# Optimization experiments

Measured on AMD Instinct MI355X. Metric: run time of the kernel, lower is better.

Reference implementation:

```python
import jax, jax.numpy as jnp
import numpy as np

B, DIM, H, W = 8, 512, 32, 32
NUM_HEADS, KEY_DIM, VALUE_DIM, DIM_OUT = 8, 64, 64, 512


def setup_inputs() -> dict:
    key = jax.random.key(0)
    ks = jax.random.split(key, 5)
    return {
        "x": jax.random.normal(ks[0], (B, DIM, H, W), dtype=jnp.float32),
        "query_proj": jax.random.normal(ks[1], (NUM_HEADS, KEY_DIM, DIM), dtype=jnp.float32),
        "key_proj": jax.random.normal(ks[2], (DIM, KEY_DIM), dtype=jnp.float32),
        "value_proj": jax.random.normal(ks[3], (DIM, VALUE_DIM), dtype=jnp.float32),
        "out_proj": jax.random.normal(ks[4], (DIM_OUT, NUM_HEADS, VALUE_DIM), dtype=jnp.float32),
    }


def reference(x, query_proj, key_proj, value_proj, out_proj):
    b, d, h, w = x.shape
    key_dim = query_proj.shape[1]
    scale = key_dim ** (-0.5)
    # flatten spatial dims to tokens: [b, n, d] where n = h*w (m == x here)
    rx = jnp.transpose(x.reshape(b, d, h * w), (0, 2, 1))
    q = jnp.einsum('bnd,hkd->bnhk', rx, query_proj)
    k = jnp.einsum('bmd,dk->bmk', rx, key_proj)          # single shared K head
    attn = jax.nn.softmax(jnp.einsum('bnhk,bmk->bnhm', q, k) * scale, axis=-1)
    v = jnp.einsum('bmd,dv->bmv', rx, value_proj)        # single shared V head
    o = jnp.einsum('bnhm,bmv->bnhv', attn, v)
    result = jnp.einsum('bnhv,dhv->bdn', o, out_proj)
    return result.reshape(b, -1, h, w)
```

## Files before the change

kernel.cpp:

```cpp
#include <hip/hip_runtime.h>
#include <math.h>

#define BATCH 8
#define DIMD  512
#define NTOK  1024
#define NH    8
#define CQKV  640
#define DOUT  512

typedef __attribute__((ext_vector_type(8))) short short8;
typedef __attribute__((ext_vector_type(4))) short short4v;
typedef __attribute__((ext_vector_type(4))) float f32x4;

__device__ __forceinline__ short bf16rn(float x) {
    unsigned u = __float_as_uint(x);
    u += 0x7FFF + ((u >> 16) & 1);
    return (short)(u >> 16);
}
__device__ __forceinline__ float bf16tof(short s) {
    return __uint_as_float(((unsigned)(unsigned short)s) << 16);
}
struct HL { short h, l; };
__device__ __forceinline__ HL bf16split(float x) {
    HL r;
    r.h = bf16rn(x);
    r.l = bf16rn(x - bf16tof(r.h));
    return r;
}
__device__ __forceinline__ void dma16(const short* g, short* l) {
    __builtin_amdgcn_global_load_lds(
        (const __attribute__((address_space(1))) unsigned int*)g,
        (__attribute__((address_space(3))) unsigned int*)l, 16, 0, 0);
}
__device__ __forceinline__ unsigned packbf2(float f0, float f1) {
    return __builtin_amdgcn_perm(__float_as_uint(f1), __float_as_uint(f0), 0x07060302);
}

#if defined(__has_builtin)
#if __has_builtin(__builtin_amdgcn_mfma_f32_16x16x16bf16_1k)
#define HAVE_MFMA16_BUILTIN 1
__device__ __forceinline__ f32x4 mfma16(short4v a, short4v b, f32x4 c) {
    return __builtin_amdgcn_mfma_f32_16x16x16bf16_1k(a, b, c, 0, 0, 0);
}
#elif __has_builtin(__builtin_amdgcn_mfma_f32_16x16x16_bf16)
#define HAVE_MFMA16_BUILTIN 1
__device__ __forceinline__ f32x4 mfma16(short4v a, short4v b, f32x4 c) {
    return __builtin_amdgcn_mfma_f32_16x16x16_bf16(a, b, c, 0, 0, 0);
}
#endif
#endif
#ifndef HAVE_MFMA16_BUILTIN
__device__ __forceinline__ f32x4 mfma16(short4v a, short4v b, f32x4 c) {
    asm("s_nop 1\n\tv_mfma_f32_16x16x16_bf16 %0, %1, %2, %0"
        : "+v"(c) : "v"(a), "v"(b));
    return c;
}
#endif


__global__ __launch_bounds__(256) void prepack_all(const float* __restrict__ x,
                                                   const float* __restrict__ qp,
                                                   const float* __restrict__ kp,
                                                   const float* __restrict__ vp,
                                                   const float* __restrict__ wout,
                                                   short* __restrict__ whi,
                                                   short* __restrict__ wlo,
                                                   short* __restrict__ xhi,
                                                   short* __restrict__ xlo,
                                                   short* __restrict__ wof) {
    __shared__ float Cs[64][65];
    const int blk = blockIdx.x;
    const int t = threadIdx.x;
    if (blk < 1024) {
        const int nt = blk & 15, dt = (blk >> 4) & 7, b = blk >> 7;
        #pragma unroll
        for (int i = 0; i < 4; ++i) {
            int row = (t >> 4) + i * 16;
            float4 v = *(const float4*)(x + ((size_t)(b * DIMD + dt * 64 + row)) * NTOK
                                          + nt * 64 + (t & 15) * 4);
            Cs[row][(t & 15) * 4 + 0] = v.x;
            Cs[row][(t & 15) * 4 + 1] = v.y;
            Cs[row][(t & 15) * 4 + 2] = v.z;
            Cs[row][(t & 15) * 4 + 3] = v.w;
        }
        __syncthreads();
        for (int u = t; u < 512; u += 256) {
            int lane2 = u & 63, cidx = u >> 6;
            int q2 = lane2 >> 4, r2 = lane2 & 15;
            int kt_loc = cidx & 1, mt_loc = cidx >> 1;
            short8 h8, l8;
            #pragma unroll
            for (int j = 0; j < 8; ++j) {
                HL s = bf16split(Cs[kt_loc * 32 + q2 * 8 + j][mt_loc * 16 + r2]);
                h8[j] = s.h; l8[j] = s.l;
            }
            size_t off = (((size_t)(b * 64 + nt * 4 + mt_loc)) * 16 + dt * 2 + kt_loc) * 512
                         + lane2 * 8;
            *(short8*)&xhi[off] = h8;
            *(short8*)&xlo[off] = l8;
        }
    } else if (blk < 1184) {
        int tid = (blk - 1024) * 256 + t;
        int lane = tid & 63, kt = (tid >> 6) & 15, ct = tid >> 10;
        int q = lane >> 4, r = lane & 15;
        int c = ct * 16 + r;
        short8 h, l;
        #pragma unroll
        for (int j = 0; j < 8; ++j) {
            int d = kt * 32 + q * 8 + j;
            float v;
            if (c < 64)       v = kp[d * 64 + c];
            else if (c < 128) v = vp[d * 64 + (c - 64)];
            else              v = qp[(size_t)(c - 128) * DIMD + d];
            HL s = bf16split(v);
            h[j] = s.h; l[j] = s.l;
        }
        *(short8*)&whi[(size_t)tid * 8] = h;
        *(short8*)&wlo[(size_t)tid * 8] = l;
    } else {
        int tid = (blk - 1184) * 256 + t;
        int lane = tid & 63, kt = (tid >> 6) & 15, mt = tid >> 10;
        int q = lane >> 4, r = lane & 15;
        const float* src = wout + (size_t)(mt * 16 + r) * DOUT + kt * 32 + q * 8;
        short8 h;
        #pragma unroll
        for (int j = 0; j < 8; ++j) h[j] = bf16rn(src[j]);
        *(short8*)&wof[(size_t)tid * 8] = h;
    }
}

__global__ __launch_bounds__(256) void qkv_gemm(const short* __restrict__ xhi,
                                                const short* __restrict__ xlo,
                                                const short* __restrict__ whi,
                                                const short* __restrict__ wlo,
                                                short* __restrict__ khi,
                                                short* __restrict__ klo,
                                                short* __restrict__ vf,
                                                short* __restrict__ qhi,
                                                short* __restrict__ qlo) {
    __shared__ __align__(16) char pool[49152];
    short* Ah = (short*)pool;
    short* Al = Ah + 8192;
    short* Bh = Al + 8192;
    short* Bl = Bh + 4096;
    float (*Cs)[65] = (float(*)[65])pool;

    const int idx = blockIdx.x;
    const int low = idx & 7, rest = idx >> 3;
    const int cb = rest % 10, gh = rest / 10;
    const int g = gh * 8 + low;
    const int b = g >> 3, bml = g & 7;

    const int tid = threadIdx.x, w = tid >> 6, lane = tid & 63;
    const int q = lane >> 4, r = lane & 15;
    f32x4 acc[2][4];
    #pragma unroll
    for (int i = 0; i < 2; ++i)
        #pragma unroll
        for (int j = 0; j < 4; ++j) acc[i][j] = (f32x4){0.f, 0.f, 0.f, 0.f};

    for (int it = 0; it < 8; ++it) {
        __syncthreads();
        for (int u = w; u < 16; u += 4) {
            size_t ga = ((size_t)((b * 64 + bml * 8 + (u >> 1)) * 16 + it * 2 + (u & 1))) * 512 + lane * 8;
            dma16(xhi + ga, &Ah[u * 512]);
            dma16(xlo + ga, &Al[u * 512]);
            if (u < 8) {
                size_t gb = ((size_t)((cb * 4 + (u >> 1)) * 16 + it * 2 + (u & 1))) * 512 + lane * 8;
                dma16(whi + gb, &Bh[u * 512]);
                dma16(wlo + gb, &Bl[u * 512]);
            }
        }
        __syncthreads();
        #pragma unroll
        for (int kc = 0; kc < 2; ++kc) {
            short8 ah[2], al[2];
            #pragma unroll
            for (int rt = 0; rt < 2; ++rt) {
                ah[rt] = *(short8*)&Ah[((w * 2 + rt) * 2 + kc) * 512 + lane * 8];
                al[rt] = *(short8*)&Al[((w * 2 + rt) * 2 + kc) * 512 + lane * 8];
            }
            #pragma unroll
            for (int tt = 0; tt < 4; ++tt) {
                short8 bh = *(short8*)&Bh[(tt * 2 + kc) * 512 + lane * 8];
                short8 bl = *(short8*)&Bl[(tt * 2 + kc) * 512 + lane * 8];
                #pragma unroll
                for (int rt = 0; rt < 2; ++rt) {
                    acc[rt][tt] = __builtin_amdgcn_mfma_f32_16x16x32_bf16(ah[rt], bh, acc[rt][tt], 0, 0, 0);
                    acc[rt][tt] = __builtin_amdgcn_mfma_f32_16x16x32_bf16(ah[rt], bl, acc[rt][tt], 0, 0, 0);
                    acc[rt][tt] = __builtin_amdgcn_mfma_f32_16x16x32_bf16(al[rt], bh, acc[rt][tt], 0, 0, 0);
                }
            }
        }
    }

    __syncthreads();
    #pragma unroll
    for (int rt = 0; rt < 2; ++rt)
        #pragma unroll
        for (int reg = 0; reg < 4; ++reg)
            #pragma unroll
            for (int tt = 0; tt < 4; ++tt)
                Cs[w * 32 + rt * 16 + q * 4 + reg][tt * 16 + r] = acc[rt][tt][reg];
    __syncthreads();

    if (cb == 0) {
        for (int u = tid; u < 1024; u += 256) {
            int lane2 = u & 63, ic = (u >> 6) & 7, tl = u >> 9;
            int q2 = lane2 >> 4, r2 = lane2 & 15;
            int i = ic >> 1, cc = ic & 1;
            short8 h8, l8;
            #pragma unroll
            for (int j = 0; j < 8; ++j) {
                HL s = bf16split(Cs[tl * 64 + i * 16 + r2][cc * 32 + q2 * 8 + j]);
                h8[j] = s.h; l8[j] = s.l;
            }
            size_t off = ((size_t)(b * 16 + bml * 2 + tl) * 8 + ic) * 512 + lane2 * 8;
            *(short8*)&khi[off] = h8;
            *(short8*)&klo[off] = l8;
        }
    } else if (cb == 1) {
        for (int u = tid; u < 1024; u += 256) {
            int lane2 = u & 63, ic = (u >> 6) & 7, tl = u >> 9;
            int q2 = lane2 >> 4, r2 = lane2 & 15;
            int tv = ic >> 1, cc = ic & 1;
            short8 v8;
            #pragma unroll
            for (int j = 0; j < 8; ++j)
                v8[j] = bf16rn(Cs[tl * 64 + cc * 32 + q2 * 8 + j][tv * 16 + r2]);
            size_t off = ((size_t)(b * 16 + bml * 2 + tl) * 8 + ic) * 512 + lane2 * 8;
            *(short8*)&vf[off] = v8;
        }
    } else {
        const int hd = cb - 2;
        const float qscale = 0.125f * 1.44269504f;
        for (int u = tid; u < 1024; u += 256) {
            int lane2 = u & 63, ch = u >> 6;
            int q2 = lane2 >> 4, r2 = lane2 & 15;
            int kc = ch & 1, ntl = ch >> 1;
            short8 h8, l8;
            #pragma unroll
            for (int j = 0; j < 8; ++j) {
                HL s = bf16split(Cs[ntl * 16 + r2][kc * 32 + q2 * 8 + j] * qscale);
                h8[j] = s.h; l8[j] = s.l;
            }
            size_t off = ((((size_t)(b * 8 + hd) * 64 + bml * 8 + ntl) * 2 + kc) * 64 + lane2) * 8;
            *(short8*)&qhi[off] = h8;
            *(short8*)&qlo[off] = l8;
        }
    }
}

__global__ __launch_bounds__(512) void attn_mfma(const short* __restrict__ qhi_g,
                                                 const short* __restrict__ qlo_g,
                                                 const short* __restrict__ khi_g,
                                                 const short* __restrict__ klo_g,
                                                 const short* __restrict__ vf_g,
                                                 short* __restrict__ ob) {
    __shared__ short Khi[2][4096], Klo[2][4096], Vf[2][4096];
    const int blk = blockIdx.x;
    const int b   = blk & 7;
    const int h   = (blk >> 3) & 7;
    const int qt  = blk >> 6;
    const int tid = threadIdx.x;
    const int w    = tid >> 6;
    const int lane = tid & 63;
    const int q    = lane >> 4;
    const int r    = lane & 15;
    const int nt = qt * 8 + w;

    short8 qhi[2], qlo[2];
    #pragma unroll
    for (int c = 0; c < 2; ++c) {
        size_t off = ((((size_t)(b * 8 + h) * 64 + nt) * 2 + c) * 64 + lane) * 8;
        qhi[c] = *(const short8*)&qhi_g[off];
        qlo[c] = *(const short8*)&qlo_g[off];
    }

    short4v bones4;
    #pragma unroll
    for (int j = 0; j < 4; ++j) bones4[j] = (short)0x3F80;

    f32x4 oacc[4], lacc;
    #pragma unroll
    for (int tt = 0; tt < 4; ++tt) oacc[tt] = (f32x4){0.f, 0.f, 0.f, 0.f};
    lacc = (f32x4){0.f, 0.f, 0.f, 0.f};
    float m_ = -1e30f;

    const int kbase = lane * 8;
    const int vbase = ((q >> 1) * 16 + r) * 8 + (q & 1) * 4;

    {
        const size_t kb = ((size_t)(b * 16 + 0) * 8) * 512;
        dma16(khi_g + kb + w * 512 + lane * 8, &Khi[0][w * 512]);
        dma16(klo_g + kb + w * 512 + lane * 8, &Klo[0][w * 512]);
        dma16(vf_g  + kb + w * 512 + lane * 8, &Vf [0][w * 512]);
    }

    for (int t = 0; t < 16; ++t) {
        const int cur = t & 1;
        __builtin_amdgcn_sched_barrier(0);
        asm volatile("s_waitcnt vmcnt(0) lgkmcnt(0)" ::: "memory");
        __builtin_amdgcn_sched_barrier(0);
        __syncthreads();
        if (t < 15) {
            const size_t kb = ((size_t)(b * 16 + t + 1) * 8) * 512;
            dma16(khi_g + kb + w * 512 + lane * 8, &Khi[cur ^ 1][w * 512]);
            dma16(klo_g + kb + w * 512 + lane * 8, &Klo[cur ^ 1][w * 512]);
            dma16(vf_g  + kb + w * 512 + lane * 8, &Vf [cur ^ 1][w * 512]);
        }

        f32x4 sT[4];
        #pragma unroll
        for (int i = 0; i < 4; ++i) sT[i] = (f32x4){0.f, 0.f, 0.f, 0.f};
        #pragma unroll
        for (int cc = 0; cc < 2; ++cc) {
            #pragma unroll
            for (int i = 0; i < 4; ++i) {
                short8 kh = *(short8*)&Khi[cur][(i * 2 + cc) * 512 + kbase];
                short8 kl = *(short8*)&Klo[cur][(i * 2 + cc) * 512 + kbase];
                sT[i] = __builtin_amdgcn_mfma_f32_16x16x32_bf16(kh, qhi[cc], sT[i], 0, 0, 0);
                sT[i] = __builtin_amdgcn_mfma_f32_16x16x32_bf16(kl, qhi[cc], sT[i], 0, 0, 0);
                sT[i] = __builtin_amdgcn_mfma_f32_16x16x32_bf16(kh, qlo[cc], sT[i], 0, 0, 0);
            }
        }

        float pm;
        {
            float a0 = fmaxf(fmaxf(sT[0][0], sT[0][1]), fmaxf(sT[0][2], sT[0][3]));
            float a1 = fmaxf(fmaxf(sT[1][0], sT[1][1]), fmaxf(sT[1][2], sT[1][3]));
            float a2 = fmaxf(fmaxf(sT[2][0], sT[2][1]), fmaxf(sT[2][2], sT[2][3]));
            float a3 = fmaxf(fmaxf(sT[3][0], sT[3][1]), fmaxf(sT[3][2], sT[3][3]));
            pm = fmaxf(fmaxf(a0, a1), fmaxf(a2, a3));
        }
        bool need = (pm > m_ + 30.f);
        if (__any((int)need)) {
            float full = fmaxf(pm, __shfl_xor(pm, 16));
            full = fmaxf(full, __shfl_xor(full, 32));
            float nm = fmaxf(m_, full);
            float alpha = exp2f(m_ - nm);
            m_ = nm;
            #pragma unroll
            for (int reg = 0; reg < 4; ++reg) {
                float areg = __shfl(alpha, q * 20 + reg);
                lacc[reg] *= areg;
                #pragma unroll
                for (int tt = 0; tt < 4; ++tt) oacc[tt][reg] *= areg;
            }
        }
        #pragma unroll
        for (int i = 0; i < 4; ++i)
            #pragma unroll
            for (int reg = 0; reg < 4; ++reg)
                sT[i][reg] = exp2f(sT[i][reg] - m_);

        #pragma unroll
        for (int c = 0; c < 4; ++c) {
            union { uint2 u; short4v s; } pk;
            pk.u.x = packbf2(sT[c][0], sT[c][1]);
            pk.u.y = packbf2(sT[c][2], sT[c][3]);
            short4v pf = pk.s;
            lacc = mfma16(pf, bones4, lacc);
            #pragma unroll
            for (int tt = 0; tt < 4; ++tt) {
                short4v vfr = *(const short4v*)
                    &Vf[cur][vbase + (tt * 2 + (c >> 1)) * 512 + (c & 1) * 256];
                oacc[tt] = mfma16(pf, vfr, oacc[tt]);
            }
        }
    }

    asm volatile("s_nop 7\n\ts_nop 7" :::);

    #pragma unroll
    for (int reg = 0; reg < 4; ++reg) {
        float inv = 1.f / lacc[reg];
        #pragma unroll
        for (int tt = 0; tt < 4; ++tt) {
            int ct = h * 2 + (tt >> 1);
            int lanep = ((tt & 1) * 2 + (r >> 3)) * 16 + q * 4 + reg;
            ob[((((size_t)b * 64 + nt) * 16 + ct) * 64 + lanep) * 8 + (r & 7)] =
                bf16rn(oacc[tt][reg] * inv);
        }
    }
}

__global__ __launch_bounds__(256) void out_gemm(const short* __restrict__ wof,
                                                const short* __restrict__ obf,
                                                float* __restrict__ out) {
    __shared__ short Ah[2][4096];
    __shared__ short Bh[2][4096];
    const int b = blockIdx.z, bd = blockIdx.y, bn = blockIdx.x;
    const int tid = threadIdx.x, w = tid >> 6, lane = tid & 63;
    const int q = lane >> 4, r = lane & 15;
    f32x4 acc[4];
    #pragma unroll
    for (int j = 0; j < 4; ++j) acc[j] = (f32x4){0.f, 0.f, 0.f, 0.f};

    for (int u = w; u < 8; u += 4) {
        size_t ga = ((size_t)((bd * 4 + (u >> 1)) * 16 + (u & 1))) * 512 + lane * 8;
        dma16(wof + ga, &Ah[0][u * 512]);
        size_t gb = ((size_t)((b * 64 + bn * 4 + (u >> 1)) * 16 + (u & 1))) * 512 + lane * 8;
        dma16(obf + gb, &Bh[0][u * 512]);
    }

    for (int it = 0; it < 8; ++it) {
        const int cur = it & 1;
        __syncthreads();
        if (it < 7) {
            for (int u = w; u < 8; u += 4) {
                size_t ga = ((size_t)((bd * 4 + (u >> 1)) * 16 + (it + 1) * 2 + (u & 1))) * 512 + lane * 8;
                dma16(wof + ga, &Ah[cur ^ 1][u * 512]);
                size_t gb = ((size_t)((b * 64 + bn * 4 + (u >> 1)) * 16 + (it + 1) * 2 + (u & 1))) * 512 + lane * 8;
                dma16(obf + gb, &Bh[cur ^ 1][u * 512]);
            }
        }
        #pragma unroll
        for (int kc = 0; kc < 2; ++kc) {
            short8 a = *(short8*)&Ah[cur][(w * 2 + kc) * 512 + lane * 8];
            #pragma unroll
            for (int tt = 0; tt < 4; ++tt) {
                short8 bb = *(short8*)&Bh[cur][(tt * 2 + kc) * 512 + lane * 8];
                acc[tt] = __builtin_amdgcn_mfma_f32_16x16x32_bf16(a, bb, acc[tt], 0, 0, 0);
            }
        }
    }
    const int d_base = bd * 64 + w * 16;
    #pragma unroll
    for (int reg = 0; reg < 4; ++reg)
        #pragma unroll
        for (int tt = 0; tt < 4; ++tt)
            out[((size_t)b * DOUT + d_base + q * 4 + reg) * NTOK
                + bn * 64 + tt * 16 + r] = acc[tt][reg];
}

extern "C" void kernel_launch(void* const* d_in, const int* in_sizes, int n_in,
                              void* d_out, int out_size, void* d_ws, size_t ws_size,
                              hipStream_t stream) {
    const float* x  = (const float*)d_in[0];
    const float* qp = (const float*)d_in[1];
    const float* kp = (const float*)d_in[2];
    const float* vp = (const float*)d_in[3];
    const float* op = (const float*)d_in[4];
    float* out = (float*)d_out;

    short* Whi = (short*)d_ws;
    short* Wlo = Whi + 327680;
    short* Xhi = Wlo + 327680;
    short* Xlo = Xhi + 4194304;
    short* Qhi = Xlo + 4194304;
    short* Qlo = Qhi + 4194304;
    short* Khi = Qlo + 4194304;
    short* Klo = Khi + 524288;
    short* Vf  = Klo + 524288;
    short* Wof = Vf  + 524288;
    short* Ob  = Xhi;

    prepack_all <<<1312, 256, 0, stream>>>(x, qp, kp, vp, op,
                                           Whi, Wlo, Xhi, Xlo, Wof);
    qkv_gemm    <<<640, 256, 0, stream>>>(Xhi, Xlo, Whi, Wlo,
                                          Khi, Klo, Vf, Qhi, Qlo);
    attn_mfma   <<<512, 512, 0, stream>>>(Qhi, Qlo, Khi, Klo, Vf, Ob);
    out_gemm    <<<dim3(16, 8, BATCH), 256, 0, stream>>>(Wof, Ob, out);
}
```

Baseline: 155.4 us.

## Process two query tiles per wave in attention and relayout V fragments

The attention kernel now uses 4 waves per block, each handling two 16-row query tiles, so every K and V fragment read from LDS is reused across two sets of MFMAs. The V prepack layout is changed to a contiguous 256-element-per-fragment format, which lets a single lane-linear short4 load feed the PV MFMA. This halves LDS traffic per unit of work and cuts block-level sync overhead. In exchange it roughly doubles accumulator register pressure, may lower occupancy, and gives each block fewer waves to hide DMA latency.

After: 159.6 us. 2.7% more time.

```diff
diff --git a/kernel.cpp b/kernel.cpp
--- a/kernel.cpp
+++ b/kernel.cpp
@@ -221,14 +221,16 @@
         }
     } else if (cb == 1) {
         for (int u = tid; u < 1024; u += 256) {
-            int lane2 = u & 63, ic = (u >> 6) & 7, tl = u >> 9;
-            int q2 = lane2 >> 4, r2 = lane2 & 15;
-            int tv = ic >> 1, cc = ic & 1;
+            int a = u & 31, ic = (u >> 5) & 15, tl = u >> 9;
+            int c4 = ic >> 2, tv = ic & 3;
             short8 v8;
             #pragma unroll
-            for (int j = 0; j < 8; ++j)
-                v8[j] = bf16rn(Cs[tl * 64 + cc * 32 + q2 * 8 + j][tv * 16 + r2]);
-            size_t off = ((size_t)(b * 16 + bml * 2 + tl) * 8 + ic) * 512 + lane2 * 8;
+            for (int jj = 0; jj < 8; ++jj) {
+                int lane2 = a * 2 + (jj >> 2), j = jj & 3;
+                int qn = lane2 >> 4, r2 = lane2 & 15;
+                v8[jj] = bf16rn(Cs[tl * 64 + c4 * 16 + qn * 4 + j][tv * 16 + r2]);
+            }
+            size_t off = ((size_t)(b * 16 + bml * 2 + tl) * 16 + ic) * 256 + a * 8;
             *(short8*)&vf[off] = v8;
         }
     } else {
@@ -251,7 +253,7 @@
     }
 }
 
-__global__ __launch_bounds__(512) void attn_mfma(const short* __restrict__ qhi_g,
+__global__ __launch_bounds__(256) void attn_mfma(const short* __restrict__ qhi_g,
                                                  const short* __restrict__ qlo_g,
                                                  const short* __restrict__ khi_g,
                                                  const short* __restrict__ klo_g,
@@ -267,34 +269,45 @@
     const int lane = tid & 63;
     const int q    = lane >> 4;
     const int r    = lane & 15;
-    const int nt = qt * 8 + w;
-
-    short8 qhi[2], qlo[2];
-    #pragma unroll
-    for (int c = 0; c < 2; ++c) {
-        size_t off = ((((size_t)(b * 8 + h) * 64 + nt) * 2 + c) * 64 + lane) * 8;
-        qhi[c] = *(const short8*)&qhi_g[off];
-        qlo[c] = *(const short8*)&qlo_g[off];
+
+    short8 qhi[2][2], qlo[2][2];
+    #pragma unroll
+    for (int rt = 0; rt < 2; ++rt) {
+        const int nt = qt * 8 + w * 2 + rt;
+        #pragma unroll
+        for (int c = 0; c < 2; ++c) {
+            size_t off = ((((size_t)(b * 8 + h) * 64 + nt) * 2 + c) * 64 + lane) * 8;
+            qhi[rt][c] = *(const short8*)&qhi_g[off];
+            qlo[rt][c] = *(const short8*)&qlo_g[off];
+        }
     }
 
     short4v bones4;
     #pragma unroll
     for (int j = 0; j < 4; ++j) bones4[j] = (short)0x3F80;
 
-    f32x4 oacc[4], lacc;
-    #pragma unroll
-    for (int tt = 0; tt < 4; ++tt) oacc[tt] = (f32x4){0.f, 0.f, 0.f, 0.f};
-    lacc = (f32x4){0.f, 0.f, 0.f, 0.f};
-    float m_ = -1e30f;
+    f32x4 oacc[2][4], lacc[2];
+    float m_[2];
+    #pragma unroll
+    for (int rt = 0; rt < 2; ++rt) {
+        #pragma unroll
+        for (int tt = 0; tt < 4; ++tt) oacc[rt][tt] = (f32x4){0.f, 0.f, 0.f, 0.f};
+        lacc[rt] = (f32x4){0.f, 0.f, 0.f, 0.f};
+        m_[rt] = -1e30f;
+    }
 
     const int kbase = lane * 8;
-    const int vbase = ((q >> 1) * 16 + r) * 8 + (q & 1) * 4;
+    const int vbase = lane * 4;
 
     {
         const size_t kb = ((size_t)(b * 16 + 0) * 8) * 512;
-        dma16(khi_g + kb + w * 512 + lane * 8, &Khi[0][w * 512]);
-        dma16(klo_g + kb + w * 512 + lane * 8, &Klo[0][w * 512]);
-        dma16(vf_g  + kb + w * 512 + lane * 8, &Vf [0][w * 512]);
+        #pragma unroll
+        for (int ch0 = 0; ch0 < 2; ++ch0) {
+            int ch = w + ch0 * 4;
+            dma16(khi_g + kb + ch * 512 + lane * 8, &Khi[0][ch * 512]);
+            dma16(klo_g + kb + ch * 512 + lane * 8, &Klo[0][ch * 512]);
+            dma16(vf_g  + kb + ch * 512 + lane * 8, &Vf [0][ch * 512]);
+        }
     }
 
     for (int t = 0; t < 16; ++t) {
@@ -305,67 +318,87 @@
         __syncthreads();
         if (t < 15) {
             const size_t kb = ((size_t)(b * 16 + t + 1) * 8) * 512;
-            dma16(khi_g + kb + w * 512 + lane * 8, &Khi[cur ^ 1][w * 512]);
-            dma16(klo_g + kb + w * 512 + lane * 8, &Klo[cur ^ 1][w * 512]);
-            dma16(vf_g  + kb + w * 512 + lane * 8, &Vf [cur ^ 1][w * 512]);
-        }
-
-        f32x4 sT[4];
-        #pragma unroll
-        for (int i = 0; i < 4; ++i) sT[i] = (f32x4){0.f, 0.f, 0.f, 0.f};
+            #pragma unroll
+            for (int ch0 = 0; ch0 < 2; ++ch0) {
+                int ch = w + ch0 * 4;
+                dma16(khi_g + kb + ch * 512 + lane * 8, &Khi[cur ^ 1][ch * 512]);
+                dma16(klo_g + kb + ch * 512 + lane * 8, &Klo[cur ^ 1][ch * 512]);
+                dma16(vf_g  + kb + ch * 512 + lane * 8, &Vf [cur ^ 1][ch * 512]);
+            }
+        }
+
+        f32x4 sT[2][4];
+        #pragma unroll
+        for (int rt = 0; rt < 2; ++rt)
+            #pragma unroll
+            for (int i = 0; i < 4; ++i) sT[rt][i] = (f32x4){0.f, 0.f, 0.f, 0.f};
         #pragma unroll
         for (int cc = 0; cc < 2; ++cc) {
             #pragma unroll
             for (int i = 0; i < 4; ++i) {
                 short8 kh = *(short8*)&Khi[cur][(i * 2 + cc) * 512 + kbase];
                 short8 kl = *(short8*)&Klo[cur][(i * 2 + cc) * 512 + kbase];
-                sT[i] = __builtin_amdgcn_mfma_f32_16x16x32_bf16(kh, qhi[cc], sT[i], 0, 0, 0);
-                sT[i] = __builtin_amdgcn_mfma_f32_16x16x32_bf16(kl, qhi[cc], sT[i], 0, 0, 0);
-                sT[i] = __builtin_amdgcn_mfma_f32_16x16x32_bf16(kh, qlo[cc], sT[i], 0, 0, 0);
-            }
-        }
-
-        float pm;
-        {
-            float a0 = fmaxf(fmaxf(sT[0][0], sT[0][1]), fmaxf(sT[0][2], sT[0][3]));
-            float a1 = fmaxf(fmaxf(sT[1][0], sT[1][1]), fmaxf(sT[1][2], sT[1][3]));
-            float a2 = fmaxf(fmaxf(sT[2][0], sT[2][1]), fmaxf(sT[2][2], sT[2][3]));
-            float a3 = fmaxf(fmaxf(sT[3][0], sT[3][1]), fmaxf(sT[3][2], sT[3][3]));
-            pm = fmaxf(fmaxf(a0, a1), fmaxf(a2, a3));
-        }
-        bool need = (pm > m_ + 30.f);
+                #pragma unroll
+                for (int rt = 0; rt < 2; ++rt) {
+                    sT[rt][i] = __builtin_amdgcn_mfma_f32_16x16x32_bf16(kh, qhi[rt][cc], sT[rt][i], 0, 0, 0);
+                    sT[rt][i] = __builtin_amdgcn_mfma_f32_16x16x32_bf16(kl, qhi[rt][cc], sT[rt][i], 0, 0, 0);
+                    sT[rt][i] = __builtin_amdgcn_mfma_f32_16x16x32_bf16(kh, qlo[rt][cc], sT[rt][i], 0, 0, 0);
+                }
+            }
+        }
+
+        float pm[2];
+        #pragma unroll
+        for (int rt = 0; rt < 2; ++rt) {
+            float a0 = fmaxf(fmaxf(sT[rt][0][0], sT[rt][0][1]), fmaxf(sT[rt][0][2], sT[rt][0][3]));
+            float a1 = fmaxf(fmaxf(sT[rt][1][0], sT[rt][1][1]), fmaxf(sT[rt][1][2], sT[rt][1][3]));
+            float a2 = fmaxf(fmaxf(sT[rt][2][0], sT[rt][2][1]), fmaxf(sT[rt][2][2], sT[rt][2][3]));
+            float a3 = fmaxf(fmaxf(sT[rt][3][0], sT[rt][3][1]), fmaxf(sT[rt][3][2], sT[rt][3][3]));
+            pm[rt] = fmaxf(fmaxf(a0, a1), fmaxf(a2, a3));
+        }
+        bool need = (pm[0] > m_[0] + 30.f) || (pm[1] > m_[1] + 30.f);
         if (__any((int)need)) {
-            float full = fmaxf(pm, __shfl_xor(pm, 16));
-            full = fmaxf(full, __shfl_xor(full, 32));
-            float nm = fmaxf(m_, full);
-            float alpha = exp2f(m_ - nm);
-            m_ = nm;
-            #pragma unroll
-            for (int reg = 0; reg < 4; ++reg) {
-                float areg = __shfl(alpha, q * 20 + reg);
-                lacc[reg] *= areg;
+            #pragma unroll
+            for (int rt = 0; rt < 2; ++rt) {
+                float full = fmaxf(pm[rt], __shfl_xor(pm[rt], 16));
+                full = fmaxf(full, __shfl_xor(full, 32));
+                float nm = fmaxf(m_[rt], full);
+                float alpha = exp2f(m_[rt] - nm);
+                m_[rt] = nm;
                 #pragma unroll
-                for (int tt = 0; tt < 4; ++tt) oacc[tt][reg] *= areg;
-            }
-        }
-        #pragma unroll
-        for (int i = 0; i < 4; ++i)
-            #pragma unroll
-            for (int reg = 0; reg < 4; ++reg)
-                sT[i][reg] = exp2f(sT[i][reg] - m_);
+                for (int reg = 0; reg < 4; ++reg) {
+                    float areg = __shfl(alpha, q * 20 + reg);
+                    lacc[rt][reg] *= areg;
+                    #pragma unroll
+                    for (int tt = 0; tt < 4; ++tt) oacc[rt][tt][reg] *= areg;
+                }
+            }
+        }
+        #pragma unroll
+        for (int rt = 0; rt < 2; ++rt)
+            #pragma unroll
+            for (int i = 0; i < 4; ++i)
+                #pragma unroll
+                for (int reg = 0; reg < 4; ++reg)
+                    sT[rt][i][reg] = exp2f(sT[rt][i][reg] - m_[rt]);
 
         #pragma unroll
         for (int c = 0; c < 4; ++c) {
-            union { uint2 u; short4v s; } pk;
-            pk.u.x = packbf2(sT[c][0], sT[c][1]);
-            pk.u.y = packbf2(sT[c][2], sT[c][3]);
-            short4v pf = pk.s;
-            lacc = mfma16(pf, bones4, lacc);
+            short4v pf[2];
+            #pragma unroll
+            for (int rt = 0; rt < 2; ++rt) {
+                union { uint2 u; short4v s; } pk;
+                pk.u.x = packbf2(sT[rt][c][0], sT[rt][c][1]);
+                pk.u.y = packbf2(sT[rt][c][2], sT[rt][c][3]);
+                pf[rt] = pk.s;
+                lacc[rt] = mfma16(pf[rt], bones4, lacc[rt]);
+            }
             #pragma unroll
             for (int tt = 0; tt < 4; ++tt) {
-                short4v vfr = *(const short4v*)
-                    &Vf[cur][vbase + (tt * 2 + (c >> 1)) * 512 + (c & 1) * 256];
-                oacc[tt] = mfma16(pf, vfr, oacc[tt]);
+                short4v vfr = *(const short4v*)&Vf[cur][(c * 4 + tt) * 256 + vbase];
+                #pragma unroll
+                for (int rt = 0; rt < 2; ++rt)
+                    oacc[rt][tt] = mfma16(pf[rt], vfr, oacc[rt][tt]);
             }
         }
     }
@@ -373,14 +406,18 @@
     asm volatile("s_nop 7\n\ts_nop 7" :::);
 
     #pragma unroll
-    for (int reg = 0; reg < 4; ++reg) {
-        float inv = 1.f / lacc[reg];
-        #pragma unroll
-        for (int tt = 0; tt < 4; ++tt) {
-            int ct = h * 2 + (tt >> 1);
-            int lanep = ((tt & 1) * 2 + (r >> 3)) * 16 + q * 4 + reg;
-            ob[((((size_t)b * 64 + nt) * 16 + ct) * 64 + lanep) * 8 + (r & 7)] =
-                bf16rn(oacc[tt][reg] * inv);
+    for (int rt = 0; rt < 2; ++rt) {
+        const int nt = qt * 8 + w * 2 + rt;
+        #pragma unroll
+        for (int reg = 0; reg < 4; ++reg) {
+            float inv = 1.f / lacc[rt][reg];
+            #pragma unroll
+            for (int tt = 0; tt < 4; ++tt) {
+                int ct = h * 2 + (tt >> 1);
+                int lanep = ((tt & 1) * 2 + (r >> 3)) * 16 + q * 4 + reg;
+                ob[((((size_t)b * 64 + nt) * 16 + ct) * 64 + lanep) * 8 + (r & 7)] =
+                    bf16rn(oacc[rt][tt][reg] * inv);
+            }
         }
     }
 }
@@ -460,6 +497,6 @@
                                            Whi, Wlo, Xhi, Xlo, Wof);
     qkv_gemm    <<<640, 256, 0, stream>>>(Xhi, Xlo, Whi, Wlo,
                                           Khi, Klo, Vf, Qhi, Qlo);
-    attn_mfma   <<<512, 512, 0, stream>>>(Qhi, Qlo, Khi, Klo, Vf, Ob);
+    attn_mfma   <<<512, 256, 0, stream>>>(Qhi, Qlo, Khi, Klo, Vf, Ob);
     out_gemm    <<<dim3(16, 8, BATCH), 256, 0, stream>>>(Wof, Ob, out);
 }
```
